# Performance work log

Hardware: AMD Instinct MI355X
Metric: run time of the kernel (lower is better)

Reference implementation:

```python
import jax, jax.numpy as jnp
import numpy as np

N_NODES = 100000
N_EDGES = 1600000
FACTOR = 0.5
REPEAT = 2


def setup_inputs() -> dict:
    key = jax.random.key(0)
    ks = jax.random.split(key, 8)
    x = jax.random.normal(ks[0], (N_NODES, 32), dtype=jnp.float32)
    edge_val = jax.random.uniform(ks[1], (N_EDGES,), dtype=jnp.float32)
    edge_row = jax.random.randint(ks[2], (N_EDGES,), 0, N_NODES)
    edge_col = jax.random.randint(ks[3], (N_EDGES,), 0, N_NODES)
    W1 = jax.random.normal(ks[4], (32, 64), dtype=jnp.float32) * 0.05
    b1 = jnp.zeros((64,), dtype=jnp.float32)
    W2 = jax.random.normal(ks[5], (64, 64), dtype=jnp.float32) * 0.05
    b2 = jnp.zeros((64,), dtype=jnp.float32)
    return {"x": x, "edge_val": edge_val, "edge_row": edge_row,
            "edge_col": edge_col, "W1": W1, "b1": b1, "W2": W2, "b2": b2}


def _spmm(edge_row, edge_col, edge_val, h):
    # out[r] += (factor * val_e) * h[c]  for each edge e=(r,c)
    gathered = (FACTOR * edge_val)[:, None] * h[edge_col]  # [E, D]
    return jax.ops.segment_sum(gathered, edge_row, num_segments=N_NODES)


def _propagate(edge_row, edge_col, edge_val, h):
    # h = (factor*A)^repeat @ h
    for _ in range(REPEAT):
        h = _spmm(edge_row, edge_col, edge_val, h)
    return h


def reference(x, edge_val, edge_row, edge_col, W1, b1, W2, b2):
    # layer 1: propagate -> linear -> relu
    h = _propagate(edge_row, edge_col, edge_val, x)
    h = jax.nn.relu(h @ W1 + b1)
    # layer 2: propagate -> linear -> identity
    h = _propagate(edge_row, edge_col, edge_val, h)
    h = h @ W2 + b2
    return h
```

## Files before the change

kernel.cpp:

```cpp
#include <hip/hip_runtime.h>
#include <hip/hip_bf16.h>


#define REGION_SHIFT 9
#define REGION_SIZE  (1 << REGION_SHIFT)
#define COL_MASK 0x1FFFF
#define GBUILD 256

typedef unsigned short u16;
typedef unsigned int   u32;
typedef __attribute__((ext_vector_type(8))) short bf16x8;
typedef __attribute__((ext_vector_type(4))) float f32x4;

__device__ inline float bflo(u32 w) { return __uint_as_float(w << 16); }
__device__ inline float bfhi(u32 w) { return __uint_as_float(w & 0xffff0000u); }
__device__ inline u32 bfpack(float a, float b) {
    u32 ua = __float_as_uint(a), ub = __float_as_uint(b);
    ua = (ua + 0x7fffu + ((ua >> 16) & 1u)) >> 16;
    ub = (ub + 0x7fffu + ((ub >> 16) & 1u)) & 0xffff0000u;
    return ua | ub;
}
__device__ inline u16 bf1(float f) {
    u32 u = __float_as_uint(f);
    return (u16)((u + 0x7fffu + ((u >> 16) & 1u)) >> 16);
}

__global__ void region_count_kernel(const int* __restrict__ er, int E,
                                    int* __restrict__ partial,
                                    const float* __restrict__ x,
                                    u16* __restrict__ xb, int n4,
                                    const float* __restrict__ W1,
                                    const float* __restrict__ W2,
                                    u16* __restrict__ W1f,
                                    u16* __restrict__ W2f) {
    for (int i = blockIdx.x * 256 + threadIdx.x; i < n4; i += gridDim.x * 256) {
        float4 a = reinterpret_cast<const float4*>(x)[i];
        uint2 o;
        o.x = bfpack(a.x, a.y);
        o.y = bfpack(a.z, a.w);
        reinterpret_cast<uint2*>(xb)[i] = o;
    }
    if (blockIdx.x == 0) {
        for (int idx = threadIdx.x; idx < 2048; idx += 256) {
            int j = idx & 7, n16 = (idx >> 3) & 15;
            int quad = (idx >> 7) & 3, t = (idx >> 9) & 3;
            W1f[idx] = bf1(W1[(quad * 8 + j) * 64 + t * 16 + n16]);
        }
        for (int idx = threadIdx.x; idx < 4096; idx += 256) {
            int j = idx & 7, n16 = (idx >> 3) & 15;
            int quad = (idx >> 7) & 3, half = (idx >> 9) & 1, t = (idx >> 10) & 3;
            W2f[idx] = bf1(W2[(half * 32 + quad * 8 + j) * 64 + t * 16 + n16]);
        }
    }
    __shared__ int hist[256];
    int t = threadIdx.x;
    hist[t] = 0;
    __syncthreads();
    int chunk = (E + gridDim.x - 1) / gridDim.x;
    int s = blockIdx.x * chunk;
    int e = min(E, s + chunk);
    for (int i = s + t; i < e; i += 256)
        atomicAdd(&hist[er[i] >> REGION_SHIFT], 1);
    __syncthreads();
    partial[blockIdx.x * 256 + t] = hist[t];
}

__global__ void region_scan_kernel(const int* __restrict__ partial,
                                   int* __restrict__ region_off,
                                   int nreg, int E, int G) {
    __shared__ int s[256];
    int t = threadIdx.x;
    int total = 0;
    if (t < nreg)
        for (int b = 0; b < G; b++) total += partial[b * 256 + t];
    s[t] = (t < nreg) ? total : 0;
    __syncthreads();
    for (int off = 1; off < 256; off <<= 1) {
        int x = (t >= off) ? s[t - off] : 0;
        __syncthreads();
        s[t] += x;
        __syncthreads();
    }
    if (t < nreg) region_off[t] = s[t] - total;
    if (t == 0) region_off[nreg] = E;
}

__global__ void region_base_kernel(int* __restrict__ partial,
                                   const int* __restrict__ region_off, int nreg) {
    __shared__ int s[256];
    int r = blockIdx.x;
    if (r >= nreg) return;
    int t = threadIdx.x;
    int c = partial[t * 256 + r];
    s[t] = c;
    __syncthreads();
    for (int off = 1; off < 256; off <<= 1) {
        int x = (t >= off) ? s[t - off] : 0;
        __syncthreads();
        s[t] += x;
        __syncthreads();
    }
    partial[t * 256 + r] = region_off[r] + s[t] - c;
}

__global__ void coarse_scatter_kernel(const int* __restrict__ er,
                                      const int* __restrict__ ec,
                                      const float* __restrict__ ev, int E,
                                      const int* __restrict__ partial,
                                      int2* __restrict__ stg) {
    __shared__ int cnt2[256], gbase[256];
    int t = threadIdx.x;
    cnt2[t] = 0;
    gbase[t] = partial[blockIdx.x * 256 + t];
    __syncthreads();
    int chunk = (E + gridDim.x - 1) / gridDim.x;
    int s0 = blockIdx.x * chunk;
    int e0 = min(E, s0 + chunk);
    for (int i = s0 + t; i < e0; i += 256) {
        int r = er[i];
        int b = r >> REGION_SHIFT;
        int rank = atomicAdd(&cnt2[b], 1);
        int2 rec;
        rec.x = ec[i] | ((r & (REGION_SIZE - 1)) << 17);
        rec.y = (int)bf1(0.5f * ev[i]);
        stg[gbase[b] + rank] = rec;
    }
}

__global__ void region_sort_kernel(const int2* __restrict__ stg,
                                   const int* __restrict__ region_off,
                                   int* __restrict__ row_ptr,
                                   u32* __restrict__ cv, int N, int E) {
    __shared__ int hist[REGION_SIZE];
    __shared__ int wp_local[REGION_SIZE];
    __shared__ int psum[256];
    int cb = blockIdx.x;
    int lo = cb << REGION_SHIFT;
    if (lo >= N) return;
    int hi = min(lo + REGION_SIZE, N);
    int cnt = hi - lo;
    int t = threadIdx.x;
    for (int r = t; r < cnt; r += 256) hist[r] = 0;
    __syncthreads();
    int start = region_off[cb];
    int end   = region_off[cb + 1];
    for (int q = start + t; q < end; q += 256)
        atomicAdd(&hist[stg[q].x >> 17], 1);
    __syncthreads();
    int a0 = (2 * t     < cnt) ? hist[2 * t]     : 0;
    int a1 = (2 * t + 1 < cnt) ? hist[2 * t + 1] : 0;
    psum[t] = a0 + a1;
    __syncthreads();
    for (int off = 1; off < 256; off <<= 1) {
        int x = (t >= off) ? psum[t - off] : 0;
        __syncthreads();
        psum[t] += x;
        __syncthreads();
    }
    int excl = psum[t] - (a0 + a1);
    if (2 * t < cnt) {
        wp_local[2 * t] = start + excl;
        row_ptr[lo + 2 * t] = start + excl;
    }
    if (2 * t + 1 < cnt) {
        wp_local[2 * t + 1] = start + excl + a0;
        row_ptr[lo + 2 * t + 1] = start + excl + a0;
    }
    if (cb == 0 && t == 0) row_ptr[N] = E;
    __syncthreads();
    for (int q = start + t; q < end; q += 256) {
        int2 e = stg[q];
        int lr = e.x >> 17;
        int p = atomicAdd(&wp_local[lr], 1);
        cv[p] = ((u32)e.y << 17) | ((u32)e.x & COL_MASK);
    }
}

__device__ inline void fma8(float acc[8], float v, uint4 w) {
    acc[0] = fmaf(v, bflo(w.x), acc[0]); acc[1] = fmaf(v, bfhi(w.x), acc[1]);
    acc[2] = fmaf(v, bflo(w.y), acc[2]); acc[3] = fmaf(v, bfhi(w.y), acc[3]);
    acc[4] = fmaf(v, bflo(w.z), acc[4]); acc[5] = fmaf(v, bfhi(w.z), acc[5]);
    acc[6] = fmaf(v, bflo(w.w), acc[6]); acc[7] = fmaf(v, bfhi(w.w), acc[7]);
}
__device__ inline float cvval(u32 q) { return __uint_as_float((q >> 17) << 16); }

template <int D, bool FINAL>
__global__ __launch_bounds__(256) void spmm_bf16_kernel(
        const u16* __restrict__ h,
        const int* __restrict__ row_ptr,
        const u32* __restrict__ cv,
        void* __restrict__ outp,
        const float* __restrict__ bias,
        int N) {
    constexpr int LPR = D / 8;
    int gid = blockIdx.x * 256 + threadIdx.x;
    int row = gid / LPR;
    int sub = gid % LPR;
    if (row >= N) return;
    int start = row_ptr[row];
    int end   = row_ptr[row + 1];
    float acc[8] = {0.f, 0.f, 0.f, 0.f, 0.f, 0.f, 0.f, 0.f};
    int j = start;
    for (; j + 4 <= end; j += 4) {
        u32 q0 = cv[j], q1 = cv[j + 1], q2 = cv[j + 2], q3 = cv[j + 3];
        uint4 w0 = reinterpret_cast<const uint4*>(h + (size_t)(q0 & COL_MASK) * D)[sub];
        uint4 w1 = reinterpret_cast<const uint4*>(h + (size_t)(q1 & COL_MASK) * D)[sub];
        uint4 w2 = reinterpret_cast<const uint4*>(h + (size_t)(q2 & COL_MASK) * D)[sub];
        uint4 w3 = reinterpret_cast<const uint4*>(h + (size_t)(q3 & COL_MASK) * D)[sub];
        fma8(acc, cvval(q0), w0);
        fma8(acc, cvval(q1), w1);
        fma8(acc, cvval(q2), w2);
        fma8(acc, cvval(q3), w3);
    }
    for (; j < end; j++) {
        u32 q = cv[j];
        uint4 w = reinterpret_cast<const uint4*>(h + (size_t)(q & COL_MASK) * D)[sub];
        fma8(acc, cvval(q), w);
    }
    if (FINAL) {
        float* op = (float*)outp + (size_t)row * 64 + sub * 8;
#pragma unroll
        for (int k = 0; k < 8; k++) acc[k] += bias[sub * 8 + k];
        reinterpret_cast<float4*>(op)[0] = make_float4(acc[0], acc[1], acc[2], acc[3]);
        reinterpret_cast<float4*>(op)[1] = make_float4(acc[4], acc[5], acc[6], acc[7]);
    } else {
        u16* ob = (u16*)outp + (size_t)row * D + sub * 8;
        uint4 o;
        o.x = bfpack(acc[0], acc[1]);
        o.y = bfpack(acc[2], acc[3]);
        o.z = bfpack(acc[4], acc[5]);
        o.w = bfpack(acc[6], acc[7]);
        reinterpret_cast<uint4*>(ob)[0] = o;
    }
}

__global__ __launch_bounds__(256) void spmm_dense_kernel(
        const u16* __restrict__ h,
        const int* __restrict__ row_ptr,
        const u32* __restrict__ cv,
        const u16* __restrict__ W1f,
        const float* __restrict__ b1,
        const u16* __restrict__ W2f,
        u16* __restrict__ outb,
        int N) {
    __shared__ __align__(16) u16 tiles[4][16][80];
    int tid = threadIdx.x;
    int lane = tid & 63;
    int wave = tid >> 6;
    int tilebase = blockIdx.x * 64 + wave * 16;
    if (tilebase >= N) return;
    int gid = blockIdx.x * 256 + tid;
    int row = gid >> 2;
    int sub = gid & 3;

    bool vr = row < N;
    int start = vr ? row_ptr[row] : 0;
    int end   = vr ? row_ptr[row + 1] : 0;
    float acc[8] = {0.f, 0.f, 0.f, 0.f, 0.f, 0.f, 0.f, 0.f};
    int j = start;
    for (; j + 4 <= end; j += 4) {
        u32 q0 = cv[j], q1 = cv[j + 1], q2 = cv[j + 2], q3 = cv[j + 3];
        uint4 w0 = reinterpret_cast<const uint4*>(h + (size_t)(q0 & COL_MASK) * 32)[sub];
        uint4 w1 = reinterpret_cast<const uint4*>(h + (size_t)(q1 & COL_MASK) * 32)[sub];
        uint4 w2 = reinterpret_cast<const uint4*>(h + (size_t)(q2 & COL_MASK) * 32)[sub];
        uint4 w3 = reinterpret_cast<const uint4*>(h + (size_t)(q3 & COL_MASK) * 32)[sub];
        fma8(acc, cvval(q0), w0);
        fma8(acc, cvval(q1), w1);
        fma8(acc, cvval(q2), w2);
        fma8(acc, cvval(q3), w3);
    }
    for (; j < end; j++) {
        u32 q = cv[j];
        uint4 w = reinterpret_cast<const uint4*>(h + (size_t)(q & COL_MASK) * 32)[sub];
        fma8(acc, cvval(q), w);
    }

    u16 (*tile)[80] = tiles[wave];
    {
        uint4 o;
        o.x = bfpack(acc[0], acc[1]);
        o.y = bfpack(acc[2], acc[3]);
        o.z = bfpack(acc[4], acc[5]);
        o.w = bfpack(acc[6], acc[7]);
        *reinterpret_cast<uint4*>(&tile[lane >> 2][sub * 8]) = o;
    }

    int n16 = lane & 15;
    int quad = lane >> 4;
    bf16x8 w1f[4];
    bf16x8 w2f[4][2];
#pragma unroll
    for (int t = 0; t < 4; t++) {
        w1f[t] = *reinterpret_cast<const bf16x8*>(&W1f[((t * 4 + quad) * 16 + n16) * 8]);
        w2f[t][0] = *reinterpret_cast<const bf16x8*>(&W2f[(((t * 2 + 0) * 4 + quad) * 16 + n16) * 8]);
        w2f[t][1] = *reinterpret_cast<const bf16x8*>(&W2f[(((t * 2 + 1) * 4 + quad) * 16 + n16) * 8]);
    }
    float b1v[4];
#pragma unroll
    for (int t = 0; t < 4; t++) b1v[t] = b1[t * 16 + n16];

    bf16x8 a1 = *reinterpret_cast<const bf16x8*>(&tile[n16][quad * 8]);
    f32x4 zero = {0.f, 0.f, 0.f, 0.f};
    f32x4 c[4];
#pragma unroll
    for (int t = 0; t < 4; t++)
        c[t] = __builtin_amdgcn_mfma_f32_16x16x32_bf16(a1, w1f[t], zero, 0, 0, 0);

#pragma unroll
    for (int t = 0; t < 4; t++)
#pragma unroll
        for (int i = 0; i < 4; i++)
            tile[quad * 4 + i][t * 16 + n16] = bf1(fmaxf(c[t][i] + b1v[t], 0.f));

    bf16x8 a2_0 = *reinterpret_cast<const bf16x8*>(&tile[n16][quad * 8]);
    bf16x8 a2_1 = *reinterpret_cast<const bf16x8*>(&tile[n16][32 + quad * 8]);
    f32x4 d[4];
#pragma unroll
    for (int t = 0; t < 4; t++) {
        d[t] = __builtin_amdgcn_mfma_f32_16x16x32_bf16(a2_0, w2f[t][0], zero, 0, 0, 0);
        d[t] = __builtin_amdgcn_mfma_f32_16x16x32_bf16(a2_1, w2f[t][1], d[t], 0, 0, 0);
    }

#pragma unroll
    for (int t = 0; t < 4; t++)
#pragma unroll
        for (int i = 0; i < 4; i++)
            tile[quad * 4 + i][t * 16 + n16] = bf1(d[t][i]);

#pragma unroll
    for (int half = 0; half < 2; half++) {
        int g = half * 512 + lane * 8;
        int r = g >> 6, cc = g & 63;
        int grow = tilebase + r;
        if (grow < N)
            *reinterpret_cast<uint4*>(outb + (size_t)grow * 64 + cc) =
                *reinterpret_cast<const uint4*>(&tile[r][cc]);
    }
}

extern "C" void kernel_launch(void* const* d_in, const int* in_sizes, int n_in,
                              void* d_out, int out_size, void* d_ws, size_t ws_size,
                              hipStream_t stream) {
    const float* x        = (const float*)d_in[0];
    const float* edge_val = (const float*)d_in[1];
    const int*   edge_row = (const int*)d_in[2];
    const int*   edge_col = (const int*)d_in[3];
    const float* W1       = (const float*)d_in[4];
    const float* b1       = (const float*)d_in[5];
    const float* W2       = (const float*)d_in[6];
    const float* b2       = (const float*)d_in[7];
    float* out = (float*)d_out;

    const int N = in_sizes[0] / 32;
    const int E = in_sizes[1];
    const int NREG = (N + REGION_SIZE - 1) >> REGION_SHIFT;

    u16* xb  = (u16*)d_out;
    u16* t0b = xb + (size_t)N * 32;
    u16* t2b = (u16*)d_out + (size_t)N * 64;

    u16*  t3b = (u16*)d_ws;
    int2* stg = (int2*)d_ws;
    int*  row_ptr    = (int*)((char*)d_ws + (size_t)N * 64 * 2);
    int*  region_off = row_ptr + (N + 1);
    int*  partial    = region_off + (NREG + 1);
    size_t wOff = (((size_t)((char*)(partial + GBUILD * 256) - (char*)d_ws)) + 15) & ~(size_t)15;
    u16* W1f = (u16*)((char*)d_ws + wOff);
    u16* W2f = W1f + 2048;
    size_t cvOff = (((size_t)((char*)(W2f + 4096) - (char*)d_ws)) + 15) & ~(size_t)15;
    u32* cv = (u32*)((char*)d_ws + cvOff);

    int n4 = (N * 32) / 4;

    region_count_kernel<<<GBUILD, 256, 0, stream>>>(edge_row, E, partial, x, xb, n4,
                                                    W1, W2, W1f, W2f);
    region_scan_kernel<<<1, 256, 0, stream>>>(partial, region_off, NREG, E, GBUILD);
    region_base_kernel<<<NREG, 256, 0, stream>>>(partial, region_off, NREG);
    coarse_scatter_kernel<<<GBUILD, 256, 0, stream>>>(edge_row, edge_col, edge_val,
                                                      E, partial, stg);
    region_sort_kernel<<<NREG, 256, 0, stream>>>(stg, region_off, row_ptr, cv, N, E);

    int g32 = (N * 4 + 255) / 256;
    int g64 = (N * 8 + 255) / 256;

    spmm_bf16_kernel<32, false><<<g32, 256, 0, stream>>>(xb, row_ptr, cv, t0b, nullptr, N);
    spmm_dense_kernel<<<g32, 256, 0, stream>>>(t0b, row_ptr, cv, W1f, b1, W2f, t2b, N);
    spmm_bf16_kernel<64, false><<<g64, 256, 0, stream>>>(t2b, row_ptr, cv, t3b, nullptr, N);
    spmm_bf16_kernel<64, true><<<g64, 256, 0, stream>>>(t3b, row_ptr, cv, out, b2, N);
}
```

Measured before the change: 298.2 us.

## Sort rows by degree within regions to balance SpMM wavefront work

Builds, inside the region sort, a per-region permutation that orders rows by degree (counting sort, capped at 63) and uses it in all SpMM kernels. Rows of similar length then share a wavefront, cutting divergence and idle lanes in the edge loops. The cost is an extra indirection load per row, scattered output writes, and extra shared-memory atomics plus a serial scan in the sort kernel.

```diff
diff --git a/kernel.cpp b/kernel.cpp
--- a/kernel.cpp
+++ b/kernel.cpp
@@ -130,10 +130,12 @@
 __global__ void region_sort_kernel(const int2* __restrict__ stg,
                                    const int* __restrict__ region_off,
                                    int* __restrict__ row_ptr,
-                                   u32* __restrict__ cv, int N, int E) {
+                                   u32* __restrict__ cv,
+                                   int* __restrict__ perm, int N, int E) {
     __shared__ int hist[REGION_SIZE];
     __shared__ int wp_local[REGION_SIZE];
     __shared__ int psum[256];
+    __shared__ int dcnt[64];
     int cb = blockIdx.x;
     int lo = cb << REGION_SHIFT;
     if (lo >= N) return;
@@ -167,7 +169,20 @@
         row_ptr[lo + 2 * t + 1] = start + excl + a0;
     }
     if (cb == 0 && t == 0) row_ptr[N] = E;
-    __syncthreads();
+    if (t < 64) dcnt[t] = 0;
+    __syncthreads();
+    for (int r = t; r < cnt; r += 256)
+        atomicAdd(&dcnt[min(hist[r], 63)], 1);
+    __syncthreads();
+    if (t == 0) {
+        int sdc = 0;
+        for (int i = 0; i < 64; i++) { int c = dcnt[i]; dcnt[i] = sdc; sdc += c; }
+    }
+    __syncthreads();
+    for (int r = t; r < cnt; r += 256) {
+        int slot = atomicAdd(&dcnt[min(hist[r], 63)], 1);
+        perm[lo + slot] = lo + r;
+    }
     for (int q = start + t; q < end; q += 256) {
         int2 e = stg[q];
         int lr = e.x >> 17;
@@ -189,14 +204,16 @@
         const u16* __restrict__ h,
         const int* __restrict__ row_ptr,
         const u32* __restrict__ cv,
+        const int* __restrict__ perm,
         void* __restrict__ outp,
         const float* __restrict__ bias,
         int N) {
     constexpr int LPR = D / 8;
     int gid = blockIdx.x * 256 + threadIdx.x;
-    int row = gid / LPR;
+    int g   = gid / LPR;
     int sub = gid % LPR;
-    if (row >= N) return;
+    if (g >= N) return;
+    int row = perm[g];
     int start = row_ptr[row];
     int end   = row_ptr[row + 1];
     float acc[8] = {0.f, 0.f, 0.f, 0.f, 0.f, 0.f, 0.f, 0.f};
@@ -238,6 +255,7 @@
         const u16* __restrict__ h,
         const int* __restrict__ row_ptr,
         const u32* __restrict__ cv,
+        const int* __restrict__ perm,
         const u16* __restrict__ W1f,
         const float* __restrict__ b1,
         const u16* __restrict__ W2f,
@@ -250,10 +268,11 @@
     int tilebase = blockIdx.x * 64 + wave * 16;
     if (tilebase >= N) return;
     int gid = blockIdx.x * 256 + tid;
-    int row = gid >> 2;
+    int g   = gid >> 2;
     int sub = gid & 3;
 
-    bool vr = row < N;
+    bool vr = g < N;
+    int row = vr ? perm[g] : 0;
     int start = vr ? row_ptr[row] : 0;
     int end   = vr ? row_ptr[row + 1] : 0;
     float acc[8] = {0.f, 0.f, 0.f, 0.f, 0.f, 0.f, 0.f, 0.f};
@@ -329,12 +348,14 @@
 
 #pragma unroll
     for (int half = 0; half < 2; half++) {
-        int g = half * 512 + lane * 8;
-        int r = g >> 6, cc = g & 63;
+        int gg = half * 512 + lane * 8;
+        int r = gg >> 6, cc = gg & 63;
         int grow = tilebase + r;
-        if (grow < N)
-            *reinterpret_cast<uint4*>(outb + (size_t)grow * 64 + cc) =
+        if (grow < N) {
+            int prow = perm[grow];
+            *reinterpret_cast<uint4*>(outb + (size_t)prow * 64 + cc) =
                 *reinterpret_cast<const uint4*>(&tile[r][cc]);
+        }
     }
 }
 
@@ -364,7 +385,8 @@
     int*  row_ptr    = (int*)((char*)d_ws + (size_t)N * 64 * 2);
     int*  region_off = row_ptr + (N + 1);
     int*  partial    = region_off + (NREG + 1);
-    size_t wOff = (((size_t)((char*)(partial + GBUILD * 256) - (char*)d_ws)) + 15) & ~(size_t)15;
+    int*  perm       = partial + GBUILD * 256;
+    size_t wOff = (((size_t)((char*)(perm + N) - (char*)d_ws)) + 15) & ~(size_t)15;
     u16* W1f = (u16*)((char*)d_ws + wOff);
     u16* W2f = W1f + 2048;
     size_t cvOff = (((size_t)((char*)(W2f + 4096) - (char*)d_ws)) + 15) & ~(size_t)15;
@@ -378,13 +400,14 @@
     region_base_kernel<<<NREG, 256, 0, stream>>>(partial, region_off, NREG);
     coarse_scatter_kernel<<<GBUILD, 256, 0, stream>>>(edge_row, edge_col, edge_val,
                                                       E, partial, stg);
-    region_sort_kernel<<<NREG, 256, 0, stream>>>(stg, region_off, row_ptr, cv, N, E);
+    region_sort_kernel<<<NREG, 256, 0, stream>>>(stg, region_off, row_ptr, cv,
+                                                 perm, N, E);
 
     int g32 = (N * 4 + 255) / 256;
     int g64 = (N * 8 + 255) / 256;
 
-    spmm_bf16_kernel<32, false><<<g32, 256, 0, stream>>>(xb, row_ptr, cv, t0b, nullptr, N);
-    spmm_dense_kernel<<<g32, 256, 0, stream>>>(t0b, row_ptr, cv, W1f, b1, W2f, t2b, N);
-    spmm_bf16_kernel<64, false><<<g64, 256, 0, stream>>>(t2b, row_ptr, cv, t3b, nullptr, N);
-    spmm_bf16_kernel<64, true><<<g64, 256, 0, stream>>>(t3b, row_ptr, cv, out, b2, N);
-}
+    spmm_bf16_kernel<32, false><<<g32, 256, 0, stream>>>(xb, row_ptr, cv, perm, t0b, nullptr, N);
+    spmm_dense_kernel<<<g32, 256, 0, stream>>>(t0b, row_ptr, cv, perm, W1f, b1, W2f, t2b, N);
+    spmm_bf16_kernel<64, false><<<g64, 256, 0, stream>>>(t2b, row_ptr, cv, perm, t3b, nullptr, N);
+    spmm_bf16_kernel<64, true><<<g64, 256, 0, stream>>>(t3b, row_ptr, cv, perm, out, b2, N);
+}
```

Result: slower. 327.5 us (+9.8%).
